# Kernel tuning notes

Hardware: AMD Instinct MI355X
Metric: run time of the kernel (lower is better)

The kernel has to match this reference:

```python
import jax, jax.numpy as jnp
import numpy as np

N = 50000      # nodes
E = 800000     # edges (no self-loops; conv adds them)
EMB = 64       # emb_dim
H = 4          # heads
C = EMB // H   # out_channels per head
L = 3          # num_layer
NEG = 0.2      # leaky_relu negative slope
EPS = 1e-5     # batchnorm eps


def setup_inputs() -> dict:
    key = jax.random.key(0)
    ks = jax.random.split(key, 12)
    x_idx = jax.random.randint(ks[0], (N,), 0, 16)
    src = jax.random.randint(ks[1], (E,), 0, N)
    off = jax.random.randint(ks[2], (E,), 1, N)
    dst = (src + off) % N  # guaranteed no self-loops
    edge_index = jnp.stack([src, dst])
    edge_attr_idx = jax.random.randint(ks[3], (E,), 0, 4)
    s = 0.1
    atom_emb = jax.random.normal(ks[4], (16, EMB)) * s
    W = jax.random.normal(ks[5], (L, EMB, H * C)) * s          # lin_src == lin_dst (shared)
    att_src = jax.random.normal(ks[6], (L, H, C)) * s
    att_dst = jax.random.normal(ks[7], (L, H, C)) * s
    att_edge = jax.random.normal(ks[8], (L, H, C)) * s
    bias = jnp.zeros((L, H * C))
    edge_emb = jax.random.normal(ks[9], (L, 4, H * C)) * s     # lin_edge embedding per layer
    bn_gamma = jnp.ones((L, EMB))
    bn_beta = jnp.zeros((L, EMB))
    pred_W = jax.random.normal(ks[10], (2 * EMB, 1)) * s
    pred_b = jnp.zeros((1,))
    return dict(x_idx=x_idx, edge_index=edge_index, edge_attr_idx=edge_attr_idx,
                atom_emb=atom_emb, W=W, att_src=att_src, att_dst=att_dst,
                att_edge=att_edge, bias=bias, edge_emb=edge_emb,
                bn_gamma=bn_gamma, bn_beta=bn_beta, pred_W=pred_W, pred_b=pred_b)


def _gat_forward(x_idx, edge_index, edge_attr_idx, atom_emb, W, att_src, att_dst,
                 att_edge, bias, edge_emb, bn_gamma, bn_beta, pred_W, pred_b):
    src, dst = edge_index[0], edge_index[1]
    loop = jnp.arange(N)
    src2 = jnp.concatenate([src, loop])   # edges + self-loops
    dst2 = jnp.concatenate([dst, loop])
    x = atom_emb[x_idx]                   # [N, EMB]
    for l in range(L):
        # embed edge attrs, self-loop fill = mean of incoming-edge features per node
        ea = edge_emb[l][edge_attr_idx]                                   # [E, H*C]
        cnt = jax.ops.segment_sum(jnp.ones((E,), ea.dtype), dst, N)       # [N]
        ea_mean = jax.ops.segment_sum(ea, dst, N) / jnp.clip(cnt, 1.0)[:, None]
        ea2 = jnp.concatenate([ea, ea_mean]).reshape(-1, H, C)            # [E+N, H, C]
        # shared src/dst projection
        xl = (x @ W[l]).reshape(N, H, C)                                  # [N, H, C]
        a_src = jnp.sum(xl * att_src[l], axis=-1)                         # [N, H]
        a_dst = jnp.sum(xl * att_dst[l], axis=-1)                         # [N, H]
        a_edge = jnp.sum(ea2 * att_edge[l], axis=-1)                      # [E+N, H]
        alpha = a_src[src2] + a_dst[dst2] + a_edge
        alpha = jnp.where(alpha >= 0, alpha, NEG * alpha)                 # leaky_relu
        # segment softmax over incoming edges of each destination node
        m = jax.ops.segment_max(alpha, dst2, N)                           # [N, H]
        ex = jnp.exp(alpha - m[dst2])
        denom = jax.ops.segment_sum(ex, dst2, N)
        alpha = ex / denom[dst2]                                          # [E+N, H]
        # message + scatter-add aggregate
        msg = alpha[:, :, None] * (xl[src2] + ea2)                        # [E+N, H, C]
        out = jax.ops.segment_sum(msg, dst2, N).reshape(N, H * C) + bias[l]
        # BatchNorm1d (training-mode batch stats, biased variance)
        mu = jnp.mean(out, axis=0)
        var = jnp.mean((out - mu) ** 2, axis=0)
        out = (out - mu) * jax.lax.rsqrt(var + EPS) * bn_gamma[l] + bn_beta[l]
        x = jax.nn.relu(out) + x                                          # residual
    pair = jnp.concatenate([x[src], x[dst]], axis=-1)                     # [E, 2*EMB]
    return pair @ pred_W + pred_b                                         # [E, 1]


def reference(x_idx, edge_index, edge_attr_idx, atom_emb, W, att_src, att_dst,
              att_edge, bias, edge_emb, bn_gamma, bn_beta, pred_W, pred_b):
    return _gat_forward(x_idx, edge_index, edge_attr_idx, atom_emb, W, att_src,
                        att_dst, att_edge, bias, edge_emb, bn_gamma, bn_beta,
                        pred_W, pred_b)
```

## Files before the change

### kernel.cpp

```cpp
#include <hip/hip_runtime.h>
#include <hip/hip_bf16.h>

#define NN 50000
#define NE 800000
#define NEG 0.2f
#define BNEPS 1e-5f
#define NB_CVT 61
#define NB_EDGE 3125
#define NB1 200
#define CH1 4000
#define NBKT 250
#define CAPBKT 4096
#define MAXS 288
#define NB_FRONT (NB_CVT + 1 + NB1)
#define NB_MID (NBKT + NN/16)

typedef __hip_bfloat16 bf16;
typedef unsigned short u16;
typedef unsigned int u32;
__device__ __forceinline__ float b2f(bf16 v){ return __bfloat162float(v); }
__device__ __forceinline__ float u2f(u16 u){ return __uint_as_float(((u32)u) << 16); }
__device__ __forceinline__ u16 f2u(float f){ bf16 b = __float2bfloat16(f); return *(u16*)&b; }

struct CvtArgs { const void* src[11]; int off[11]; int cnt[11]; };

__global__ __launch_bounds__(256) void k_front(CvtArgs a, const void* eeraw,
        const void* aeraw, const int* __restrict__ src, const int* __restrict__ dst,
        const int* __restrict__ ety,
        float* __restrict__ cw, float* __restrict__ aet, int* __restrict__ flag,
        int* __restrict__ bcur, u32* __restrict__ bins){
  int t = threadIdx.x, b = blockIdx.x;
  if (b >= NB_CVT + 1){
    __shared__ int cnt[NBKT], start[NBKT], cur[NBKT];
    __shared__ int dcache[CH1];
    int bb = b - (NB_CVT + 1);
    for (int i = t; i < NBKT; i += 256){ cnt[i] = 0; cur[i] = 0; }
    __syncthreads();
    int base = bb*CH1;
    for (int k = t; k < CH1; k += 256){
      int d = dst[base + k];
      dcache[k] = d;
      atomicAdd(&cnt[(u32)d/200u], 1);
    }
    __syncthreads();
    for (int i = t; i < NBKT; i += 256) start[i] = atomicAdd(&bcur[i], cnt[i]);
    __syncthreads();
    for (int k = t; k < CH1; k += 256){
      int e = base + k;
      u32 d = (u32)dcache[k];
      u32 bk = d/200u;
      int pos = start[bk] + atomicAdd(&cur[bk], 1);
      if (pos < CAPBKT)
        bins[bk*CAPBKT + pos] = (u32)src[e] | ((u32)ety[e] << 16) | ((d - bk*200u) << 18);
    }
    return;
  }
  __shared__ int sflag;
  if (t < 64){
    const u16* u = (const u16*)a.src[0];
    int hit = 0;
    for (int i = t; i < 512; i += 64){
      int ex = (u[i] >> 7) & 0xFF;
      if (ex >= 0x8A || (ex != 0 && ex <= 0x60)) hit = 1;
    }
    unsigned long long bl = __ballot(hit);
    if (t == 0) sflag = (bl != 0ULL) ? 1 : 0;
  }
  __syncthreads();
  int f = sflag;
  if (b == 0 && t == 0) *flag = f;
  if (b < NB_CVT){
    int i = b*256 + t;
    #pragma unroll
    for (int s = 0; s < 11; ++s){
      int j = i - a.off[s];
      if (j >= 0 && j < a.cnt[s])
        cw[a.off[s] + j] = f ? ((const float*)a.src[s])[j]
                             : b2f(((const bf16*)a.src[s])[j]);
    }
  } else if (t < 48){
    int l = t >> 4, ty = (t >> 2) & 3, h = t & 3;
    float s = 0.f;
    for (int cc = 0; cc < 16; ++cc){
      int ei = l*256 + ty*64 + h*16 + cc;
      int ai = l*64 + h*16 + cc;
      float ev = f ? ((const float*)eeraw)[ei] : b2f(((const bf16*)eeraw)[ei]);
      float av = f ? ((const float*)aeraw)[ai] : b2f(((const bf16*)aeraw)[ai]);
      s += ev*av;
    }
    aet[t] = s;
  }
}

__global__ __launch_bounds__(256) void k_mid(const int* __restrict__ bcur,
        const u32* __restrict__ bins,
        int* __restrict__ cpack, int* __restrict__ rowst, int* __restrict__ cnt4,
        const int* __restrict__ xidx, const float* __restrict__ aembf,
        const float* __restrict__ Wl, const float* __restrict__ att_s,
        const float* __restrict__ att_d,
        float* __restrict__ x, u16* __restrict__ bxl,
        float* __restrict__ asrc, float* __restrict__ adst){
  __shared__ __align__(16) char smem[17408];
  int t = threadIdx.x, b = blockIdx.x;
  if (b < NBKT){
    int* c4   = (int*)smem;
    int* nst  = c4 + 800;
    int* ncur = nst + 200;
    int* bco  = ncur + 200;
    int* s    = bco + 256;
    for (int i = t; i < 800; i += 256) c4[i] = 0;
    if (t < 200) ncur[t] = 0;
    int v = 0;
    if (t < NBKT){ v = bcur[t]; if (v > CAPBKT) v = CAPBKT; }
    bco[t] = v; s[t] = v;
    __syncthreads();
    for (int o = 1; o < 256; o <<= 1){
      int a2 = s[t]; int add = (t >= o) ? s[t-o] : 0;
      __syncthreads(); s[t] = a2 + add; __syncthreads();
    }
    int gb = s[b] - bco[b];
    int tot = bco[b];
    int total = s[255];
    __syncthreads();
    for (int i = t; i < tot; i += 256){
      u32 e = bins[b*CAPBKT + i];
      atomicAdd(&c4[((e >> 18) & 0xFF)*4 + ((e >> 16) & 3)], 1);
    }
    __syncthreads();
    int deg = 0;
    if (t < 200) deg = c4[t*4] + c4[t*4+1] + c4[t*4+2] + c4[t*4+3];
    s[t] = deg; __syncthreads();
    for (int o = 1; o < 256; o <<= 1){
      int a2 = s[t]; int add = (t >= o) ? s[t-o] : 0;
      __syncthreads(); s[t] = a2 + add; __syncthreads();
    }
    if (t < 200) nst[t] = s[t] - deg;
    __syncthreads();
    if (t < 200){
      int n = b*200 + t;
      rowst[n] = gb + nst[t];
      *(int4*)&cnt4[n*4] = make_int4(c4[t*4], c4[t*4+1], c4[t*4+2], c4[t*4+3]);
    }
    if (b == 0 && t == 0) rowst[NN] = total;
    for (int i = t; i < tot; i += 256){
      u32 e = bins[b*CAPBKT + i];
      int nl = (e >> 18) & 0xFF;
      int pos = nst[nl] + atomicAdd(&ncur[nl], 1);
      cpack[gb + pos] = (int)(e & 0x3FFFF);
    }
    return;
  }
  float* Ws = (float*)smem;
  float* xs = Ws + 4096;
  int bp = b - NBKT;
  for (int i = t; i < 4096; i += 256) Ws[i] = Wl[i];
  int c = t & 63, wv = t >> 6;
  float ats = att_s[c], atd = att_d[c];
  for (int pass = 0; pass < 4; ++pass){
    int n = bp*16 + pass*4 + wv;
    float xv = aembf[xidx[n]*64 + c];
    x[n*64 + c] = xv;
    __syncthreads();
    xs[t] = xv;
    __syncthreads();
    const float* xr = &xs[wv*64];
    float acc = 0.f;
    #pragma unroll
    for (int k = 0; k < 64; ++k) acc += xr[k]*Ws[k*64 + c];
    bxl[n*64 + c] = f2u(acc);
    float vs = acc*ats, vd = acc*atd;
    #pragma unroll
    for (int o = 8; o >= 1; o >>= 1){ vs += __shfl_xor(vs,o,64); vd += __shfl_xor(vd,o,64); }
    if ((c & 15) == 0){ asrc[n*4 + (c>>4)] = vs; adst[n*4 + (c>>4)] = vd; }
  }
}

__global__ __launch_bounds__(256) void k_bnproj(
    const float* __restrict__ opre, const float* __restrict__ bnred,
    const float* __restrict__ gam, const float* __restrict__ bet,
    const float* __restrict__ Wl,
    const float* __restrict__ att_s, const float* __restrict__ att_d,
    float* __restrict__ x, u16* __restrict__ bxl,
    float* __restrict__ asrc, float* __restrict__ adst){
  __shared__ float Ws[4096];
  __shared__ float xs[256];
  int t = threadIdx.x;
  for (int i = t; i < 4096; i += 256) Ws[i] = Wl[i];
  int c = t & 63, wv = t >> 6;
  float mu  = bnred[c] * (1.f/NN);
  float var = bnred[64+c] * (1.f/NN) - mu*mu;
  float rstd = rsqrtf(var + BNEPS);
  float g = gam[c], be = bet[c];
  float ats = att_s[c], atd = att_d[c];
  for (int pass = 0; pass < 4; ++pass){
    int n = blockIdx.x*16 + pass*4 + wv;
    float o = (opre[n*64 + c] - mu)*rstd*g + be;
    float xv = x[n*64 + c] + fmaxf(o, 0.f);
    x[n*64 + c] = xv;
    __syncthreads();
    xs[t] = xv;
    __syncthreads();
    const float* xr = &xs[wv*64];
    float acc = 0.f;
    #pragma unroll
    for (int k = 0; k < 64; ++k) acc += xr[k]*Ws[k*64 + c];
    bxl[n*64 + c] = f2u(acc);
    float vs = acc*ats, vd = acc*atd;
    #pragma unroll
    for (int o2 = 8; o2 >= 1; o2 >>= 1){ vs += __shfl_xor(vs,o2,64); vd += __shfl_xor(vd,o2,64); }
    if ((c & 15) == 0){ asrc[n*4 + (c>>4)] = vs; adst[n*4 + (c>>4)] = vd; }
  }
}

__global__ __launch_bounds__(256) void k_aggr(
    const u16* __restrict__ bxl,
    const float* __restrict__ asrc, const float* __restrict__ adst,
    const int* __restrict__ cnt4, const int* __restrict__ rowst,
    const int* __restrict__ cpack,
    const float* __restrict__ eeg, const float* __restrict__ aetg,
    const float* __restrict__ biasg,
    float* __restrict__ opre, float* __restrict__ bnpart){
  __shared__ float ee[256];
  __shared__ float aetL[16];
  __shared__ float adl[32];
  __shared__ float4 wsh[MAXS];
  __shared__ int ents[MAXS];
  __shared__ float redA[256], redB[256];
  __shared__ int rs[9];
  int t = threadIdx.x;
  int n0 = blockIdx.x*8;
  ee[t] = eeg[t];
  if (t < 16) aetL[t] = aetg[t];
  if (t >= 32 && t < 64) adl[t-32] = adst[n0*4 + (t-32)];
  if (t >= 64 && t < 73) rs[t-64] = rowst[n0 + (t-64)];
  __syncthreads();
  int jb0 = rs[0], je0 = rs[8], cnt = je0 - jb0;
  int lim = cnt < MAXS ? cnt : MAXS;
  for (int s = t; s < lim; s += 256){
    int j = jb0 + s;
    int pk = cpack[j];
    ents[s] = pk;
    int sr = pk & 0xFFFF, ty = pk >> 16;
    int dl = (j>=rs[1])+(j>=rs[2])+(j>=rs[3])+(j>=rs[4])+(j>=rs[5])+(j>=rs[6])+(j>=rs[7]);
    float4 as4 = *(const float4*)&asrc[sr*4];
    float a0 = as4.x + adl[dl*4+0] + aetL[ty*4+0]; a0 = a0>=0.f ? a0 : NEG*a0;
    float a1 = as4.y + adl[dl*4+1] + aetL[ty*4+1]; a1 = a1>=0.f ? a1 : NEG*a1;
    float a2 = as4.z + adl[dl*4+2] + aetL[ty*4+2]; a2 = a2>=0.f ? a2 : NEG*a2;
    float a3 = as4.w + adl[dl*4+3] + aetL[ty*4+3]; a3 = a3>=0.f ? a3 : NEG*a3;
    wsh[s] = make_float4(__expf(a0), __expf(a1), __expf(a2), __expf(a3));
  }
  __syncthreads();
  int wv = t >> 6, c = t & 63, h = c >> 4;
  const float* wshf = (const float*)wsh;
  float sA = 0.f, sB = 0.f;
  #pragma unroll
  for (int half = 0; half < 2; ++half){
    int node = wv + half*4;
    int n = n0 + node;
    int jb = rs[node], je = rs[node+1];
    int4 c4 = *(const int4*)&cnt4[n*4];
    int deg = c4.x + c4.y + c4.z + c4.w;
    float inv = 1.f / (float)(deg > 0 ? deg : 1);
    float eam = ((float)c4.x*ee[c] + (float)c4.y*ee[64+c]
               + (float)c4.z*ee[128+c] + (float)c4.w*ee[192+c]) * inv;
    float aes = ((float)c4.x*aetL[h] + (float)c4.y*aetL[4+h]
               + (float)c4.z*aetL[8+h] + (float)c4.w*aetL[12+h]) * inv;
    float adn = adl[node*4 + h];
    float a = asrc[n*4 + h] + adn + aes;
    a = a >= 0.f ? a : NEG*a;
    float wself = __expf(a);
    float den = wself;
    float acc = wself * (u2f(bxl[n*64 + c]) + eam);
    int jlim = jb0 + lim;
    int jeP = je < jlim ? je : jlim;
    int j = jb;
    for (; j + 8 <= jeP; j += 8){
      int so = j - jb0;
      int pk0 = ents[so],   pk1 = ents[so+1], pk2 = ents[so+2], pk3 = ents[so+3];
      int pk4 = ents[so+4], pk5 = ents[so+5], pk6 = ents[so+6], pk7 = ents[so+7];
      float w0 = wshf[(so  )*4 + h], w1 = wshf[(so+1)*4 + h];
      float w2 = wshf[(so+2)*4 + h], w3 = wshf[(so+3)*4 + h];
      float w4 = wshf[(so+4)*4 + h], w5 = wshf[(so+5)*4 + h];
      float w6 = wshf[(so+6)*4 + h], w7 = wshf[(so+7)*4 + h];
      float x0 = u2f(bxl[(pk0&0xFFFF)*64 + c]), x1 = u2f(bxl[(pk1&0xFFFF)*64 + c]);
      float x2 = u2f(bxl[(pk2&0xFFFF)*64 + c]), x3 = u2f(bxl[(pk3&0xFFFF)*64 + c]);
      float x4 = u2f(bxl[(pk4&0xFFFF)*64 + c]), x5 = u2f(bxl[(pk5&0xFFFF)*64 + c]);
      float x6 = u2f(bxl[(pk6&0xFFFF)*64 + c]), x7 = u2f(bxl[(pk7&0xFFFF)*64 + c]);
      acc += w0*(x0 + ee[(pk0>>16)*64 + c]); den += w0;
      acc += w1*(x1 + ee[(pk1>>16)*64 + c]); den += w1;
      acc += w2*(x2 + ee[(pk2>>16)*64 + c]); den += w2;
      acc += w3*(x3 + ee[(pk3>>16)*64 + c]); den += w3;
      acc += w4*(x4 + ee[(pk4>>16)*64 + c]); den += w4;
      acc += w5*(x5 + ee[(pk5>>16)*64 + c]); den += w5;
      acc += w6*(x6 + ee[(pk6>>16)*64 + c]); den += w6;
      acc += w7*(x7 + ee[(pk7>>16)*64 + c]); den += w7;
    }
    for (; j + 4 <= jeP; j += 4){
      int so = j - jb0;
      int pk0 = ents[so], pk1 = ents[so+1], pk2 = ents[so+2], pk3 = ents[so+3];
      float w0 = wshf[(so  )*4 + h], w1 = wshf[(so+1)*4 + h];
      float w2 = wshf[(so+2)*4 + h], w3 = wshf[(so+3)*4 + h];
      float x0 = u2f(bxl[(pk0&0xFFFF)*64 + c]), x1 = u2f(bxl[(pk1&0xFFFF)*64 + c]);
      float x2 = u2f(bxl[(pk2&0xFFFF)*64 + c]), x3 = u2f(bxl[(pk3&0xFFFF)*64 + c]);
      acc += w0*(x0 + ee[(pk0>>16)*64 + c]); den += w0;
      acc += w1*(x1 + ee[(pk1>>16)*64 + c]); den += w1;
      acc += w2*(x2 + ee[(pk2>>16)*64 + c]); den += w2;
      acc += w3*(x3 + ee[(pk3>>16)*64 + c]); den += w3;
    }
    for (; j < jeP; ++j){
      int pk = ents[j - jb0];
      float wj = wshf[(j - jb0)*4 + h];
      acc += wj*(u2f(bxl[(pk&0xFFFF)*64 + c]) + ee[(pk>>16)*64 + c]); den += wj;
    }
    for (; j < je; ++j){
      int pk = cpack[j];
      int s_ = pk & 0xFFFF, ty = pk >> 16;
      float aa = asrc[s_*4 + h] + adn + aetL[ty*4 + h];
      aa = aa >= 0.f ? aa : NEG*aa;
      float wj = __expf(aa);
      acc += wj*(u2f(bxl[s_*64 + c]) + ee[ty*64 + c]); den += wj;
    }
    float out = acc/den + biasg[c];
    opre[n*64 + c] = out;
    sA += out; sB += out*out;
  }
  redA[t] = sA; redB[t] = sB;
  __syncthreads();
  int part = blockIdx.x & 127;
  if (t < 64){
    atomicAdd(&bnpart[part*128 + t], redA[t]+redA[64+t]+redA[128+t]+redA[192+t]);
  } else if (t < 128){
    int cc = t - 64;
    atomicAdd(&bnpart[part*128 + 64 + cc], redB[cc]+redB[64+cc]+redB[128+cc]+redB[192+cc]);
  }
}

__global__ __launch_bounds__(1024) void k_bnstat(float* __restrict__ bnpart,
                                                 float* __restrict__ bnred){
  __shared__ float red[1024];
  int t = threadIdx.x;
  int c = t & 127, g = t >> 7;
  float s = 0.f;
  for (int p = g; p < 128; p += 8){ s += bnpart[p*128 + c]; bnpart[p*128 + c] = 0.f; }
  red[g*128 + c] = s; __syncthreads();
  if (t < 128){
    float tot = 0.f;
    #pragma unroll
    for (int g2 = 0; g2 < 8; ++g2) tot += red[g2*128 + t];
    bnred[t] = tot;
  }
}

__global__ __launch_bounds__(256) void k_bnpred(
    const float* __restrict__ x, const float* __restrict__ opre,
    const float* __restrict__ bnred, const float* __restrict__ gam,
    const float* __restrict__ bet, const float* __restrict__ pW,
    float* __restrict__ s1, float* __restrict__ s2){
  int t = threadIdx.x, wv = t >> 6, c = t & 63;
  int n = blockIdx.x*4 + wv;
  float mu  = bnred[c] * (1.f/NN);
  float var = bnred[64+c] * (1.f/NN) - mu*mu;
  float o = (opre[n*64 + c] - mu)*rsqrtf(var + BNEPS)*gam[c] + bet[c];
  float xv = x[n*64 + c] + fmaxf(o, 0.f);
  float v1 = xv*pW[c], v2 = xv*pW[64 + c];
  #pragma unroll
  for (int o2 = 32; o2 >= 1; o2 >>= 1){ v1 += __shfl_xor(v1,o2,64); v2 += __shfl_xor(v2,o2,64); }
  if (c == 0){ s1[n] = v1; s2[n] = v2; }
}

__global__ void k_pred_edge(const int* __restrict__ src, const int* __restrict__ dst,
        const float* __restrict__ s1, const float* __restrict__ s2,
        const float* __restrict__ pbf, const int* __restrict__ flag, void* out){
  int e = blockIdx.x*256 + threadIdx.x;
  if (e < NE){
    float v = s1[src[e]] + s2[dst[e]] + pbf[0];
    if (*flag) ((float*)out)[e] = v;
    else       ((bf16*)out)[e] = __float2bfloat16(v);
  }
}

extern "C" void kernel_launch(void* const* d_in, const int* in_sizes, int n_in,
                              void* d_out, int out_size, void* d_ws, size_t ws_size,
                              hipStream_t stream){
  const int*  xidx = (const int*)d_in[0];
  const int*  eidx = (const int*)d_in[1];
  const int*  ety  = (const int*)d_in[2];
  const int* srcp = eidx, *dstp = eidx + NE;

  float* p = (float*)d_ws;
  float* x      = p;            p += NN*64;
  float* opre   = p;            p += NN*64;
  float* asrc   = p;            p += NN*4;
  float* adst   = p;            p += NN*4;
  float* bnred  = p;            p += 128;
  float* s1     = p;            p += NN;
  float* s2     = p;            p += NN;
  float* cw     = p;            p += 15392;
  float* aet    = p;            p += 64;
  float* bnpart = p;            p += 128*128;
  int*   bcur   = (int*)p;
  char*  zend   = (char*)(bcur + 256);
  size_t zbytes = (size_t)(zend - (char*)bnpart);
  u32*   bins   = (u32*)(bcur + 256);
  int*   cpack  = (int*)(bins + NBKT*CAPBKT);
  int*   rowst  = cpack + NE;
  int*   cnt4   = rowst + NN + 4;
  int*   flag   = cnt4 + NN*4;
  u16*   bxl    = (u16*)(flag + 4);

  const int O_AEMB = 0,     N_AEMB = 1024;
  const int O_W    = 1024,  N_W    = 12288;
  const int O_AS   = 13312, N_AS   = 192;
  const int O_AD   = 13504, N_AD   = 192;
  const int O_AE   = 13696, N_AE   = 192;
  const int O_BI   = 13888, N_BI   = 192;
  const int O_EE   = 14080, N_EE   = 768;
  const int O_GA   = 14848, N_GA   = 192;
  const int O_BE   = 15040, N_BE   = 192;
  const int O_PW   = 15232, N_PW   = 128;
  const int O_PB   = 15360, N_PB   = 1;

  CvtArgs ca;
  ca.src[0]=d_in[3];  ca.off[0]=O_AEMB; ca.cnt[0]=N_AEMB;
  ca.src[1]=d_in[4];  ca.off[1]=O_W;    ca.cnt[1]=N_W;
  ca.src[2]=d_in[5];  ca.off[2]=O_AS;   ca.cnt[2]=N_AS;
  ca.src[3]=d_in[6];  ca.off[3]=O_AD;   ca.cnt[3]=N_AD;
  ca.src[4]=d_in[7];  ca.off[4]=O_AE;   ca.cnt[4]=N_AE;
  ca.src[5]=d_in[8];  ca.off[5]=O_BI;   ca.cnt[5]=N_BI;
  ca.src[6]=d_in[9];  ca.off[6]=O_EE;   ca.cnt[6]=N_EE;
  ca.src[7]=d_in[10]; ca.off[7]=O_GA;   ca.cnt[7]=N_GA;
  ca.src[8]=d_in[11]; ca.off[8]=O_BE;   ca.cnt[8]=N_BE;
  ca.src[9]=d_in[12]; ca.off[9]=O_PW;   ca.cnt[9]=N_PW;
  ca.src[10]=d_in[13];ca.off[10]=O_PB;  ca.cnt[10]=N_PB;

  hipMemsetAsync(bnpart, 0, zbytes, stream);
  k_front<<<NB_FRONT, 256, 0, stream>>>(ca, d_in[9], d_in[7], srcp, dstp, ety,
                                        cw, aet, flag, bcur, bins);
  k_mid<<<NB_MID, 256, 0, stream>>>(bcur, bins, cpack, rowst, cnt4,
                                    xidx, cw + O_AEMB, cw + O_W,
                                    cw + O_AS, cw + O_AD, x, bxl, asrc, adst);
  for (int l = 0; l < 3; ++l){
    k_aggr<<<NN/8, 256, 0, stream>>>(bxl, asrc, adst, cnt4, rowst, cpack,
                                     cw + O_EE + l*256, aet + l*16,
                                     cw + O_BI + l*64, opre, bnpart);
    k_bnstat<<<1, 1024, 0, stream>>>(bnpart, bnred);
    if (l < 2)
      k_bnproj<<<NN/16, 256, 0, stream>>>(opre, bnred, cw + O_GA + l*64,
                                          cw + O_BE + l*64, cw + O_W + (l+1)*4096,
                                          cw + O_AS + (l+1)*64, cw + O_AD + (l+1)*64,
                                          x, bxl, asrc, adst);
  }
  k_bnpred<<<NN/4, 256, 0, stream>>>(x, opre, bnred, cw + O_GA + 128,
                                     cw + O_BE + 128, cw + O_PW, s1, s2);
  k_pred_edge<<<NB_EDGE, 256, 0, stream>>>(srcp, dstp, s1, s2, cw + O_PB, flag, d_out);
}
```

Measured before the change: 251.1 us.

## Fold BN stat reduction into consumers and deepen gather unroll in aggregation

Removes the single-block k_bnstat kernel launched after each layer. Consumer kernels (k_bnproj, k_bnpred) now reduce NPARTS=32 partial-sum slots themselves, and each layer writes to its own buffer, so no re-zeroing pass is needed. The number of atomic partitions drops from 128 to 32, which makes the redundant per-block reduction cheap but raises atomic contention. The aggregation loop adds a 16-wide unrolled gather with two accumulators to keep more loads in flight, at some register-pressure risk. The workspace is also realigned to 256 bytes.

```diff
diff --git a/kernel.cpp b/kernel.cpp
--- a/kernel.cpp
+++ b/kernel.cpp
@@ -12,6 +12,7 @@
 #define NBKT 250
 #define CAPBKT 4096
 #define MAXS 288
+#define NPARTS 32
 #define NB_FRONT (NB_CVT + 1 + NB1)
 #define NB_MID (NBKT + NN/16)
 
@@ -176,7 +177,7 @@
 }
 
 __global__ __launch_bounds__(256) void k_bnproj(
-    const float* __restrict__ opre, const float* __restrict__ bnred,
+    const float* __restrict__ opre, const float* __restrict__ bnp,
     const float* __restrict__ gam, const float* __restrict__ bet,
     const float* __restrict__ Wl,
     const float* __restrict__ att_s, const float* __restrict__ att_d,
@@ -184,11 +185,22 @@
     float* __restrict__ asrc, float* __restrict__ adst){
   __shared__ float Ws[4096];
   __shared__ float xs[256];
+  __shared__ float sred[256];
+  __shared__ float stat[128];
   int t = threadIdx.x;
+  {
+    int cc = t & 127;
+    float s = 0.f;
+    for (int p2 = t >> 7; p2 < NPARTS; p2 += 2) s += bnp[p2*128 + cc];
+    sred[t] = s;
+  }
   for (int i = t; i < 4096; i += 256) Ws[i] = Wl[i];
+  __syncthreads();
+  if (t < 128) stat[t] = sred[t] + sred[128 + t];
+  __syncthreads();
   int c = t & 63, wv = t >> 6;
-  float mu  = bnred[c] * (1.f/NN);
-  float var = bnred[64+c] * (1.f/NN) - mu*mu;
+  float mu  = stat[c] * (1.f/NN);
+  float var = stat[64+c] * (1.f/NN) - mu*mu;
   float rstd = rsqrtf(var + BNEPS);
   float g = gam[c], be = bet[c];
   float ats = att_s[c], atd = att_d[c];
@@ -219,7 +231,7 @@
     const int* __restrict__ cpack,
     const float* __restrict__ eeg, const float* __restrict__ aetg,
     const float* __restrict__ biasg,
-    float* __restrict__ opre, float* __restrict__ bnpart){
+    float* __restrict__ opre, float* __restrict__ bnp){
   __shared__ float ee[256];
   __shared__ float aetL[16];
   __shared__ float adl[32];
@@ -274,26 +286,30 @@
     int jlim = jb0 + lim;
     int jeP = je < jlim ? je : jlim;
     int j = jb;
+    for (; j + 16 <= jeP; j += 16){
+      int so = j - jb0;
+      int pk[16]; float w[16], xv[16];
+      #pragma unroll
+      for (int q = 0; q < 16; ++q){ pk[q] = ents[so+q]; w[q] = wshf[(so+q)*4 + h]; }
+      #pragma unroll
+      for (int q = 0; q < 16; ++q) xv[q] = u2f(bxl[(pk[q]&0xFFFF)*64 + c]);
+      float accB = 0.f, denB = 0.f;
+      #pragma unroll
+      for (int q = 0; q < 16; ++q){
+        if (q & 1){ accB += w[q]*(xv[q] + ee[(pk[q]>>16)*64 + c]); denB += w[q]; }
+        else      { acc  += w[q]*(xv[q] + ee[(pk[q]>>16)*64 + c]); den  += w[q]; }
+      }
+      acc += accB; den += denB;
+    }
     for (; j + 8 <= jeP; j += 8){
       int so = j - jb0;
-      int pk0 = ents[so],   pk1 = ents[so+1], pk2 = ents[so+2], pk3 = ents[so+3];
-      int pk4 = ents[so+4], pk5 = ents[so+5], pk6 = ents[so+6], pk7 = ents[so+7];
-      float w0 = wshf[(so  )*4 + h], w1 = wshf[(so+1)*4 + h];
-      float w2 = wshf[(so+2)*4 + h], w3 = wshf[(so+3)*4 + h];
-      float w4 = wshf[(so+4)*4 + h], w5 = wshf[(so+5)*4 + h];
-      float w6 = wshf[(so+6)*4 + h], w7 = wshf[(so+7)*4 + h];
-      float x0 = u2f(bxl[(pk0&0xFFFF)*64 + c]), x1 = u2f(bxl[(pk1&0xFFFF)*64 + c]);
-      float x2 = u2f(bxl[(pk2&0xFFFF)*64 + c]), x3 = u2f(bxl[(pk3&0xFFFF)*64 + c]);
-      float x4 = u2f(bxl[(pk4&0xFFFF)*64 + c]), x5 = u2f(bxl[(pk5&0xFFFF)*64 + c]);
-      float x6 = u2f(bxl[(pk6&0xFFFF)*64 + c]), x7 = u2f(bxl[(pk7&0xFFFF)*64 + c]);
-      acc += w0*(x0 + ee[(pk0>>16)*64 + c]); den += w0;
-      acc += w1*(x1 + ee[(pk1>>16)*64 + c]); den += w1;
-      acc += w2*(x2 + ee[(pk2>>16)*64 + c]); den += w2;
-      acc += w3*(x3 + ee[(pk3>>16)*64 + c]); den += w3;
-      acc += w4*(x4 + ee[(pk4>>16)*64 + c]); den += w4;
-      acc += w5*(x5 + ee[(pk5>>16)*64 + c]); den += w5;
-      acc += w6*(x6 + ee[(pk6>>16)*64 + c]); den += w6;
-      acc += w7*(x7 + ee[(pk7>>16)*64 + c]); den += w7;
+      int pk[8]; float w[8], xv[8];
+      #pragma unroll
+      for (int q = 0; q < 8; ++q){ pk[q] = ents[so+q]; w[q] = wshf[(so+q)*4 + h]; }
+      #pragma unroll
+      for (int q = 0; q < 8; ++q) xv[q] = u2f(bxl[(pk[q]&0xFFFF)*64 + c]);
+      #pragma unroll
+      for (int q = 0; q < 8; ++q){ acc += w[q]*(xv[q] + ee[(pk[q]>>16)*64 + c]); den += w[q]; }
     }
     for (; j + 4 <= jeP; j += 4){
       int so = j - jb0;
@@ -326,40 +342,36 @@
   }
   redA[t] = sA; redB[t] = sB;
   __syncthreads();
-  int part = blockIdx.x & 127;
+  int part = blockIdx.x & (NPARTS-1);
   if (t < 64){
-    atomicAdd(&bnpart[part*128 + t], redA[t]+redA[64+t]+redA[128+t]+redA[192+t]);
+    atomicAdd(&bnp[part*128 + t], redA[t]+redA[64+t]+redA[128+t]+redA[192+t]);
   } else if (t < 128){
     int cc = t - 64;
-    atomicAdd(&bnpart[part*128 + 64 + cc], redB[cc]+redB[64+cc]+redB[128+cc]+redB[192+cc]);
-  }
-}
-
-__global__ __launch_bounds__(1024) void k_bnstat(float* __restrict__ bnpart,
-                                                 float* __restrict__ bnred){
-  __shared__ float red[1024];
-  int t = threadIdx.x;
-  int c = t & 127, g = t >> 7;
-  float s = 0.f;
-  for (int p = g; p < 128; p += 8){ s += bnpart[p*128 + c]; bnpart[p*128 + c] = 0.f; }
-  red[g*128 + c] = s; __syncthreads();
-  if (t < 128){
-    float tot = 0.f;
-    #pragma unroll
-    for (int g2 = 0; g2 < 8; ++g2) tot += red[g2*128 + t];
-    bnred[t] = tot;
+    atomicAdd(&bnp[part*128 + 64 + cc], redB[cc]+redB[64+cc]+redB[128+cc]+redB[192+cc]);
   }
 }
 
 __global__ __launch_bounds__(256) void k_bnpred(
     const float* __restrict__ x, const float* __restrict__ opre,
-    const float* __restrict__ bnred, const float* __restrict__ gam,
+    const float* __restrict__ bnp, const float* __restrict__ gam,
     const float* __restrict__ bet, const float* __restrict__ pW,
     float* __restrict__ s1, float* __restrict__ s2){
-  int t = threadIdx.x, wv = t >> 6, c = t & 63;
+  __shared__ float sred[256];
+  __shared__ float stat[128];
+  int t = threadIdx.x;
+  {
+    int cc = t & 127;
+    float s = 0.f;
+    for (int p2 = t >> 7; p2 < NPARTS; p2 += 2) s += bnp[p2*128 + cc];
+    sred[t] = s;
+  }
+  __syncthreads();
+  if (t < 128) stat[t] = sred[t] + sred[128 + t];
+  __syncthreads();
+  int wv = t >> 6, c = t & 63;
   int n = blockIdx.x*4 + wv;
-  float mu  = bnred[c] * (1.f/NN);
-  float var = bnred[64+c] * (1.f/NN) - mu*mu;
+  float mu  = stat[c] * (1.f/NN);
+  float var = stat[64+c] * (1.f/NN) - mu*mu;
   float o = (opre[n*64 + c] - mu)*rsqrtf(var + BNEPS)*gam[c] + bet[c];
   float xv = x[n*64 + c] + fmaxf(o, 0.f);
   float v1 = xv*pW[c], v2 = xv*pW[64 + c];
@@ -387,26 +399,28 @@
   const int*  ety  = (const int*)d_in[2];
   const int* srcp = eidx, *dstp = eidx + NE;
 
-  float* p = (float*)d_ws;
-  float* x      = p;            p += NN*64;
-  float* opre   = p;            p += NN*64;
-  float* asrc   = p;            p += NN*4;
-  float* adst   = p;            p += NN*4;
-  float* bnred  = p;            p += 128;
-  float* s1     = p;            p += NN;
-  float* s2     = p;            p += NN;
-  float* cw     = p;            p += 15392;
-  float* aet    = p;            p += 64;
-  float* bnpart = p;            p += 128*128;
-  int*   bcur   = (int*)p;
-  char*  zend   = (char*)(bcur + 256);
-  size_t zbytes = (size_t)(zend - (char*)bnpart);
-  u32*   bins   = (u32*)(bcur + 256);
-  int*   cpack  = (int*)(bins + NBKT*CAPBKT);
-  int*   rowst  = cpack + NE;
-  int*   cnt4   = rowst + NN + 4;
-  int*   flag   = cnt4 + NN*4;
-  u16*   bxl    = (u16*)(flag + 4);
+  char* base = (char*)d_ws;
+  auto alloc = [&](size_t bytes) -> char* {
+    char* r = base; base += (bytes + 255) & ~(size_t)255; return r;
+  };
+  float* x      = (float*)alloc(NN*64*4);
+  float* opre   = (float*)alloc(NN*64*4);
+  float* asrc   = (float*)alloc(NN*4*4);
+  float* adst   = (float*)alloc(NN*4*4);
+  float* s1     = (float*)alloc(NN*4);
+  float* s2     = (float*)alloc(NN*4);
+  float* cw     = (float*)alloc(15392*4);
+  float* aet    = (float*)alloc(64*4);
+  char*  zchunk = alloc(3*NPARTS*128*4 + 256*4);
+  float* bnpart = (float*)zchunk;
+  int*   bcur   = (int*)(zchunk + 3*NPARTS*128*4);
+  size_t zbytes = 3*NPARTS*128*4 + 256*4;
+  u32*   bins   = (u32*)alloc((size_t)NBKT*CAPBKT*4);
+  int*   cpack  = (int*)alloc(NE*4);
+  int*   rowst  = (int*)alloc((NN+4)*4);
+  int*   cnt4   = (int*)alloc(NN*4*4);
+  int*   flag   = (int*)alloc(256);
+  u16*   bxl    = (u16*)alloc(NN*64*2);
 
   const int O_AEMB = 0,     N_AEMB = 1024;
   const int O_W    = 1024,  N_W    = 12288;
@@ -433,7 +447,7 @@
   ca.src[9]=d_in[12]; ca.off[9]=O_PW;   ca.cnt[9]=N_PW;
   ca.src[10]=d_in[13];ca.off[10]=O_PB;  ca.cnt[10]=N_PB;
 
-  hipMemsetAsync(bnpart, 0, zbytes, stream);
+  hipMemsetAsync(zchunk, 0, zbytes, stream);
   k_front<<<NB_FRONT, 256, 0, stream>>>(ca, d_in[9], d_in[7], srcp, dstp, ety,
                                         cw, aet, flag, bcur, bins);
   k_mid<<<NB_MID, 256, 0, stream>>>(bcur, bins, cpack, rowst, cnt4,
@@ -442,15 +456,16 @@
   for (int l = 0; l < 3; ++l){
     k_aggr<<<NN/8, 256, 0, stream>>>(bxl, asrc, adst, cnt4, rowst, cpack,
                                      cw + O_EE + l*256, aet + l*16,
-                                     cw + O_BI + l*64, opre, bnpart);
-    k_bnstat<<<1, 1024, 0, stream>>>(bnpart, bnred);
+                                     cw + O_BI + l*64, opre, bnpart + l*NPARTS*128);
     if (l < 2)
-      k_bnproj<<<NN/16, 256, 0, stream>>>(opre, bnred, cw + O_GA + l*64,
-                                          cw + O_BE + l*64, cw + O_W + (l+1)*4096,
+      k_bnproj<<<NN/16, 256, 0, stream>>>(opre, bnpart + l*NPARTS*128,
+                                          cw + O_GA + l*64, cw + O_BE + l*64,
+                                          cw + O_W + (l+1)*4096,
                                           cw + O_AS + (l+1)*64, cw + O_AD + (l+1)*64,
                                           x, bxl, asrc, adst);
   }
-  k_bnpred<<<NN/4, 256, 0, stream>>>(x, opre, bnred, cw + O_GA + 128,
-                                     cw + O_BE + 128, cw + O_PW, s1, s2);
+  k_bnpred<<<NN/4, 256, 0, stream>>>(x, opre, bnpart + 2*NPARTS*128,
+                                     cw + O_GA + 128, cw + O_BE + 128,
+                                     cw + O_PW, s1, s2);
   k_pred_edge<<<NB_EDGE, 256, 0, stream>>>(srcp, dstp, s1, s2, cw + O_PB, flag, d_out);
 }
```

Result: slower. 295.5 us (+17.7%).
